# Kernel optimization log

Hardware: AMD Instinct MI355X
Metric: run time of the kernel (lower is better)

Reference implementation:

```python
import jax, jax.numpy as jnp
import numpy as np

NUM_TAGS = 128
VOCAB = 50257
SEQ_LEN = 8192
START_TAG = 0   # tag2id['<s>'] in the original
END_TAG = 1     # vocab['</s>'] in the original (code quirk; treated as end-tag id)
NEG_INF = -10000.0


def setup_inputs() -> dict:
    key = jax.random.key(0)
    k1, k2, k3 = jax.random.split(key, 3)
    x = jax.random.randint(k1, (SEQ_LEN,), 0, VOCAB)
    emit_score = jax.random.normal(k2, (VOCAB, NUM_TAGS), dtype=jnp.float32)
    transitions = jax.random.normal(k3, (NUM_TAGS, NUM_TAGS), dtype=jnp.float32)
    return {"x": x, "emit_score": emit_score, "transitions": transitions}


def reference(x, emit_score, transitions):
    # CRF forward algorithm (log partition function z).
    # Original: per-timestep, per-tag python loops of log_sum_exp over
    # _score = alphas[:, None] + emit[ch_id][None, :] + transitions.
    # All num_tags updates at step t read the *old* alphas (the in-place
    # writes only touch _score's source after it was built), so this is the
    # standard vectorized recurrence: a logsumexp reduction over the prev-tag axis.
    emits = emit_score[x[1:]]  # [S-1, T] gathered emission scores
    init_alphas = jnp.full((NUM_TAGS,), NEG_INF, dtype=emit_score.dtype).at[START_TAG].set(0.0)

    def step(alphas, emit_t):
        # score[prev, cur] = alphas[prev] + emit_t[cur] + transitions[prev, cur]
        score = alphas[:, None] + emit_t[None, :] + transitions  # [T, T]
        return jax.nn.logsumexp(score, axis=0), None

    alphas, _ = jax.lax.scan(step, init_alphas, emits)
    z = jax.nn.logsumexp(alphas + transitions[:, END_TAG])  # scalar
    return z
```

## Files before the change

### kernel.cpp

```cpp
#include <hip/hip_runtime.h>

#define NTG 128
#define NSTEPS 8191
#define GCH 512
#define LCH 16
#define MATF16 (NTG*NTG)

typedef _Float16 half8v  __attribute__((ext_vector_type(8)));
typedef _Float16 half4v  __attribute__((ext_vector_type(4)));
typedef float    float4v __attribute__((ext_vector_type(4)));

__device__ __forceinline__ int su(int row, int col){
  return (row*NTG + col) ^ ((row & 15) << 3);
}

__device__ __forceinline__ float wave_max(float v){
#pragma unroll
  for (int m = 32; m >= 1; m >>= 1) v = fmaxf(v, __shfl_xor(v, m));
  return v;
}
__device__ __forceinline__ float wave_sum(float v){
#pragma unroll
  for (int m = 32; m >= 1; m >>= 1) v += __shfl_xor(v, m);
  return v;
}

__device__ __forceinline__ float red8(const float* rg){
  const float4v r0 = *(const float4v*)rg;
  const float4v r1 = *(const float4v*)(rg+4);
  return fmaxf(fmaxf(fmaxf(r0[0],r0[1]),fmaxf(r0[2],r0[3])),
               fmaxf(fmaxf(r1[0],r1[1]),fmaxf(r1[2],r1[3])));
}

__global__ __launch_bounds__(512, 4)
void k_chunks(const int* __restrict__ x, const float* __restrict__ emit,
              const float* __restrict__ T, _Float16* __restrict__ Pt,
              double* __restrict__ scale)
{
  __shared__ _Float16 X[2][MATF16];
  __shared__ float ehl[2][NTG];
  __shared__ float red_g[2][8];

  const int t = threadIdx.x, lane = t & 63, wv = t >> 6;
  const int l15 = lane & 15, g4 = lane >> 4;
  const int wr = wv >> 1, wc = wv & 1;
  const int g = blockIdx.x, s0 = g*LCH;
  const int nst = min(LCH, NSTEPS - s0);

  half8v aE[2][4];
#pragma unroll
  for (int rt=0; rt<2; ++rt){
    const int j = wr*32 + rt*16 + l15;
#pragma unroll
    for (int ks=0; ks<4; ++ks){
      half8v a;
#pragma unroll
      for (int jj=0; jj<8; ++jj)
        a[jj] = (_Float16)__expf(T[(ks*32 + g4*8 + jj)*NTG + j]);
      aE[rt][ks] = a;
    }
  }

  int tokv = 0;
  if (wv==0) tokv = x[1 + s0 + min(lane, nst-1)];

  double cacc = 0.0;
  {
    const int tok0 = x[1+s0];
    const float2 e0 = *(const float2*)(emit + (size_t)tok0*NTG + lane*2);
    const float m0 = wave_max(fmaxf(e0.x, e0.y));
    const float sa = __expf(e0.x - m0)*0.0078125f;
    const float sb = __expf(e0.y - m0)*0.0078125f;
    const int j0 = lane*2;
#pragma unroll
    for (int it=0; it<16; ++it){
      const int idx = it*512 + t;
      const int i = idx >> 6;
      const float2 tv = *(const float2*)(T + (size_t)i*NTG + j0);
      union { unsigned u; _Float16 h[2]; } pk;
      pk.h[0] = (_Float16)(__expf(tv.x)*sa);
      pk.h[1] = (_Float16)(__expf(tv.y)*sb);
      *(unsigned*)&X[1][su(i, j0)] = pk.u;
    }
    if (t==0) cacc = (double)m0 + 4.852030263919617;
    if (wv==0){
      const int tok1 = __shfl(tokv, 1);
      const float2 e1 = *(const float2*)(emit + (size_t)tok1*NTG + lane*2);
      const float m1 = wave_max(fmaxf(e1.x, e1.y));
      *(float2*)&ehl[1][lane*2] = make_float2(__expf(e1.x-m1), __expf(e1.y-m1));
      if (t==0) cacc += (double)m1;
    }
    if (t<8) red_g[0][t] = 1.0f;
  }

  float4v accv[2][4];
  for (int s=1; s<nst; ++s){
    __syncthreads();
    const float gmax = red8(&red_g[(s-1)&1][0]);
    const float pscale = 1.0f/gmax;
    if (t==0) cacc += (double)__logf(gmax);

#pragma unroll
    for (int rt=0;rt<2;++rt)
#pragma unroll
      for (int ct=0;ct<4;++ct) accv[rt][ct] = (float4v){0.f,0.f,0.f,0.f};

    const _Float16* __restrict__ Xs = X[s&1];
#pragma unroll
    for (int ct=0; ct<4; ++ct){
      const int c = wc*64 + ct*16 + l15;
      half8v bf[4];
#pragma unroll
      for (int ks=0;ks<4;++ks)
        bf[ks] = *(const half8v*)&Xs[su(c, ks*32 + g4*8)];
#pragma unroll
      for (int rt=0;rt<2;++rt)
#pragma unroll
        for (int ks=0;ks<4;++ks)
          accv[rt][ct] = __builtin_amdgcn_mfma_f32_16x16x32_f16(aE[rt][ks], bf[ks], accv[rt][ct], 0,0,0);
    }

    if (wv==0 && s+1<nst){
      const int tokn = __shfl(tokv, s+1);
      const float2 en = *(const float2*)(emit + (size_t)tokn*NTG + lane*2);
      const float mn = wave_max(fmaxf(en.x,en.y));
      *(float2*)&ehl[(s+1)&1][lane*2] = make_float2(__expf(en.x-mn), __expf(en.y-mn));
      if (t==0) cacc += (double)mn;
    }

    float gm = 0.f;
    _Float16* __restrict__ Xd = X[(s+1)&1];
#pragma unroll
    for (int rt=0;rt<2;++rt){
      const float4v eh4 = *(const float4v*)&ehl[s&1][wr*32 + rt*16 + g4*4];
#pragma unroll
      for (int ct=0;ct<4;++ct){
        half4v h;
#pragma unroll
        for (int r=0;r<4;r++){
          const float v = accv[rt][ct][r]*eh4[r]*pscale;
          gm = fmaxf(gm, v);
          h[r] = (_Float16)v;
        }
        *(half4v*)&Xd[su(wc*64 + ct*16 + l15, wr*32 + rt*16 + g4*4)] = h;
      }
    }
    gm = wave_max(gm);
    if (lane==0) red_g[s&1][wv] = gm;
  }

  __syncthreads();
  {
    const float gmaxF = red8(&red_g[(nst-1)&1][0]);
    const float inv = 1.0f/gmaxF;
    const _Float16* __restrict__ Xf = X[nst&1];
    unsigned* pt = (unsigned*)(Pt + (size_t)g*MATF16);
#pragma unroll
    for (int it=0; it<16; ++it){
      const int uidx = it*512 + t;
      const int jj = uidx >> 6, ii = (uidx & 63)*2;
      union { unsigned u; _Float16 h[2]; } pk;
      pk.h[0] = (_Float16)((float)Xf[su(ii,   jj)]*inv);
      pk.h[1] = (_Float16)((float)Xf[su(ii+1, jj)]*inv);
      pt[uidx] = pk.u;
    }
    if (t==0) scale[g] = cacc + (double)__logf(gmaxF);
  }
}

__global__ __launch_bounds__(512, 2)
void k_comb8(const _Float16* __restrict__ Pt_in, const double* __restrict__ Sin,
             _Float16* __restrict__ Pt_out, double* __restrict__ Sout)
{
  __shared__ _Float16 X[2][MATF16];
  __shared__ float red_g[2][8];
  const int t = threadIdx.x, lane = t & 63, wv = t >> 6;
  const int l15 = lane & 15, g4 = lane >> 4;
  const int wr = wv >> 1, wc = wv & 1;
  const int p = blockIdx.x;
  const _Float16* __restrict__ base = Pt_in + (size_t)p*8*MATF16;

  {
    const unsigned* src = (const unsigned*)base;
#pragma unroll
    for (int it=0; it<16; ++it){
      const int pos = it*512 + t;
      union { unsigned u; _Float16 h[2]; } pk;
      pk.u = src[pos];
      const int jj = pos >> 6, ii = (pos & 63)*2;
      X[1][su(ii,   jj)] = pk.h[0];
      X[1][su(ii+1, jj)] = pk.h[1];
    }
    if (t<8) red_g[0][t] = 1.0f;
  }

  half8v aB[2][4];
#pragma unroll
  for (int rt=0;rt<2;++rt)
#pragma unroll
    for (int ks=0;ks<4;++ks)
      aB[rt][ks] = *(const half8v*)(base + MATF16 + (size_t)(wr*32+rt*16+l15)*NTG + ks*32 + g4*8);

  double slog = 0.0;
  float4v accv[2][4];
#pragma unroll
  for (int mi=1; mi<8; ++mi){
    __syncthreads();
    const float gmax = red8(&red_g[(mi-1)&1][0]);
    const float pscale = 1.0f/gmax;
    if (t==0) slog += (double)__logf(gmax);

#pragma unroll
    for (int rt=0;rt<2;++rt)
#pragma unroll
      for (int ct=0;ct<4;++ct) accv[rt][ct] = (float4v){0.f,0.f,0.f,0.f};

    const _Float16* __restrict__ Xs = X[mi&1];
#pragma unroll
    for (int ct=0; ct<4; ++ct){
      const int c = wc*64 + ct*16 + l15;
      half8v bf[4];
#pragma unroll
      for (int ks=0;ks<4;++ks)
        bf[ks] = *(const half8v*)&Xs[su(c, ks*32 + g4*8)];
#pragma unroll
      for (int rt=0;rt<2;++rt)
#pragma unroll
        for (int ks=0;ks<4;++ks)
          accv[rt][ct] = __builtin_amdgcn_mfma_f32_16x16x32_f16(aB[rt][ks], bf[ks], accv[rt][ct], 0,0,0);
    }

    half8v aBn[2][4];
    if (mi<7){
#pragma unroll
      for (int rt=0;rt<2;++rt)
#pragma unroll
        for (int ks=0;ks<4;++ks)
          aBn[rt][ks] = *(const half8v*)(base + (size_t)(mi+1)*MATF16 + (size_t)(wr*32+rt*16+l15)*NTG + ks*32 + g4*8);
    }

    float gm = 0.f;
    _Float16* __restrict__ Xd = X[(mi+1)&1];
#pragma unroll
    for (int rt=0;rt<2;++rt)
#pragma unroll
      for (int ct=0;ct<4;++ct){
        half4v h;
#pragma unroll
        for (int r=0;r<4;r++){
          const float v = accv[rt][ct][r]*pscale;
          gm = fmaxf(gm, v);
          h[r] = (_Float16)v;
        }
        *(half4v*)&Xd[su(wc*64 + ct*16 + l15, wr*32 + rt*16 + g4*4)] = h;
      }
    gm = wave_max(gm);
    if (lane==0) red_g[mi&1][wv] = gm;

    if (mi<7){
#pragma unroll
      for (int rt=0;rt<2;++rt)
#pragma unroll
        for (int ks=0;ks<4;++ks) aB[rt][ks] = aBn[rt][ks];
    }
  }

  __syncthreads();
  {
    const float gmaxF = red8(&red_g[1][0]);
    const float inv = 1.0f/gmaxF;
    const _Float16* __restrict__ Xf = X[0];
    unsigned* pt = (unsigned*)(Pt_out + (size_t)p*MATF16);
#pragma unroll
    for (int it=0; it<16; ++it){
      const int uidx = it*512 + t;
      const int jj = uidx >> 6, ii = (uidx & 63)*2;
      union { unsigned u; _Float16 h[2]; } pk;
      pk.h[0] = (_Float16)((float)Xf[su(ii,   jj)]*inv);
      pk.h[1] = (_Float16)((float)Xf[su(ii+1, jj)]*inv);
      pt[uidx] = pk.u;
    }
    if (t==0){
      double ssum = slog + (double)__logf(gmaxF);
#pragma unroll
      for (int q=0;q<8;q++) ssum += Sin[p*8+q];
      Sout[p] = ssum;
    }
  }
}

__global__ void k_final(const _Float16* __restrict__ PtC, const double* __restrict__ scC,
                        const float* __restrict__ T, float* __restrict__ out)
{
  __shared__ float u[2][NTG];
  __shared__ float red[4], red2[4];
  const int t = threadIdx.x;
  const int lane = t & 63, wv = t >> 6;

  double acc = 0.0;
#pragma unroll
  for (int q=0;q<8;q++) acc += scC[q];

  if (t < NTG) u[0][t] = (t==0) ? 1.f : 0.f;
  __syncthreads();

  int cur = 0;
  const int r = t >> 1, off = (t&1)*64;
  for (int k=0;k<8;k++){
    const _Float16* Y = PtC + (size_t)k*MATF16 + (size_t)r*NTG + off;
    float dot = 0.f;
#pragma unroll
    for (int q=0;q<8;q++){
      const half8v h = *(const half8v*)(Y + q*8);
#pragma unroll
      for (int e=0;e<8;e++) dot += (float)h[e]*u[cur][off + q*8 + e];
    }
    dot += __shfl_xor(dot, 1);
    if ((t&1)==0) u[cur^1][r] = dot;
    __syncthreads();
    cur ^= 1;
  }

  const float val = (t < NTG) ? (__logf(u[cur][t]) + T[t*NTG + 1]) : -3.0e38f;
  float mx = wave_max(val);
  if (lane==0) red[wv] = mx;
  __syncthreads();
  mx = fmaxf(red[0], red[1]);
  const float e = (t < NTG) ? __expf(val - mx) : 0.f;
  const float s = wave_sum(e);
  if (lane==0) red2[wv] = s;
  __syncthreads();
  if (t==0){
    const double z = (double)mx + log((double)(red2[0]+red2[1])) + acc;
    out[0] = (float)z;
  }
}

extern "C" void kernel_launch(void* const* d_in, const int* in_sizes, int n_in,
                              void* d_out, int out_size, void* d_ws, size_t ws_size,
                              hipStream_t stream)
{
  const int*   x    = (const int*)d_in[0];
  const float* emit = (const float*)d_in[1];
  const float* T    = (const float*)d_in[2];
  float* out = (float*)d_out;

  _Float16* PtA = (_Float16*)d_ws;
  _Float16* PtB = PtA + (size_t)512*MATF16;
  _Float16* PtC = PtB + (size_t)64*MATF16;
  double* scA = (double*)(PtC + (size_t)8*MATF16);
  double* scB = scA + 512;
  double* scC = scB + 64;

  k_chunks<<<GCH, 512, 0, stream>>>(x, emit, T, PtA, scA);
  k_comb8<<<64, 512, 0, stream>>>(PtA, scA, PtB, scB);
  k_comb8<<< 8, 512, 0, stream>>>(PtB, scB, PtC, scC);
  k_final<<<1, 256, 0, stream>>>(PtC, scC, T, out);
}
```

Measured before the change: 171.9 us.

## Restructure CRF scan: more shorter chunks, precomputed exp(T), single-buffer LDS, deeper final chain

Doubles the number of chunk blocks and halves steps per chunk. exp(transitions) is now computed once in a prep kernel, in normal and transposed fp16 form, instead of per block. LDS drops to a single buffer with an extra barrier, and the warp tiling changes to 2x4 so each wave holds 4 A-row tiles. Launch bounds target 8 blocks per CU. One comb8 level is removed, and the final kernel now runs a 128-step matrix-vector chain with per-step max normalization and prefetching. The aim is more parallelism and less redundant exp work, at the cost of a longer serial final reduction and an extra synchronization per step.

Measured after the change: 555.0 us. 223% more time.

```diff
diff --git a/kernel.cpp b/kernel.cpp
--- a/kernel.cpp
+++ b/kernel.cpp
@@ -2,9 +2,10 @@
 
 #define NTG 128
 #define NSTEPS 8191
-#define GCH 512
-#define LCH 16
+#define GCH 1024
+#define LCH 8
 #define MATF16 (NTG*NTG)
+#define NB1 (GCH/8)
 
 typedef _Float16 half8v  __attribute__((ext_vector_type(8)));
 typedef _Float16 half4v  __attribute__((ext_vector_type(4)));
@@ -24,7 +25,6 @@
   for (int m = 32; m >= 1; m >>= 1) v += __shfl_xor(v, m);
   return v;
 }
-
 __device__ __forceinline__ float red8(const float* rg){
   const float4v r0 = *(const float4v*)rg;
   const float4v r1 = *(const float4v*)(rg+4);
@@ -32,292 +32,302 @@
                fmaxf(fmaxf(r1[0],r1[1]),fmaxf(r1[2],r1[3])));
 }
 
-__global__ __launch_bounds__(512, 4)
+__global__ void k_prep(const float* __restrict__ T, _Float16* __restrict__ En,
+                       _Float16* __restrict__ Et){
+  const int idx = blockIdx.x*256 + threadIdx.x;
+  const int i = idx >> 7, j = idx & 127;
+  const float v = __expf(T[idx]);
+  En[idx] = (_Float16)v;
+  Et[j*NTG + i] = (_Float16)v;
+}
+
+__global__ __launch_bounds__(512, 8)
 void k_chunks(const int* __restrict__ x, const float* __restrict__ emit,
-              const float* __restrict__ T, _Float16* __restrict__ Pt,
-              double* __restrict__ scale)
+              const _Float16* __restrict__ En, const _Float16* __restrict__ Et,
+              _Float16* __restrict__ Pt, double* __restrict__ scale)
 {
-  __shared__ _Float16 X[2][MATF16];
-  __shared__ float ehl[2][NTG];
+  __shared__ _Float16 X[MATF16];
   __shared__ float red_g[2][8];
 
   const int t = threadIdx.x, lane = t & 63, wv = t >> 6;
   const int l15 = lane & 15, g4 = lane >> 4;
-  const int wr = wv >> 1, wc = wv & 1;
+  const int wr = wv >> 2, wc = wv & 3;
   const int g = blockIdx.x, s0 = g*LCH;
   const int nst = min(LCH, NSTEPS - s0);
 
-  half8v aE[2][4];
-#pragma unroll
-  for (int rt=0; rt<2; ++rt){
-    const int j = wr*32 + rt*16 + l15;
-#pragma unroll
-    for (int ks=0; ks<4; ++ks){
-      half8v a;
-#pragma unroll
-      for (int jj=0; jj<8; ++jj)
-        a[jj] = (_Float16)__expf(T[(ks*32 + g4*8 + jj)*NTG + j]);
-      aE[rt][ks] = a;
-    }
-  }
-
-  int tokv = 0;
-  if (wv==0) tokv = x[1 + s0 + min(lane, nst-1)];
+  half8v aE[4][4];
+#pragma unroll
+  for (int rt=0; rt<4; ++rt){
+    const int j = wr*64 + rt*16 + l15;
+#pragma unroll
+    for (int ks=0; ks<4; ++ks)
+      aE[rt][ks] = *(const half8v*)(Et + j*NTG + ks*32 + g4*8);
+  }
+
+  const int tokv = x[1 + s0 + min(lane & 7, nst-1)];
 
   double cacc = 0.0;
   {
-    const int tok0 = x[1+s0];
+    const int tok0 = __shfl(tokv, 0);
     const float2 e0 = *(const float2*)(emit + (size_t)tok0*NTG + lane*2);
     const float m0 = wave_max(fmaxf(e0.x, e0.y));
     const float sa = __expf(e0.x - m0)*0.0078125f;
     const float sb = __expf(e0.y - m0)*0.0078125f;
     const int j0 = lane*2;
+    const unsigned* ens = (const unsigned*)En;
 #pragma unroll
     for (int it=0; it<16; ++it){
       const int idx = it*512 + t;
       const int i = idx >> 6;
-      const float2 tv = *(const float2*)(T + (size_t)i*NTG + j0);
       union { unsigned u; _Float16 h[2]; } pk;
-      pk.h[0] = (_Float16)(__expf(tv.x)*sa);
-      pk.h[1] = (_Float16)(__expf(tv.y)*sb);
-      *(unsigned*)&X[1][su(i, j0)] = pk.u;
+      pk.u = ens[idx];
+      pk.h[0] = (_Float16)((float)pk.h[0]*sa);
+      pk.h[1] = (_Float16)((float)pk.h[1]*sb);
+      *(unsigned*)&X[su(i, j0)] = pk.u;
     }
     if (t==0) cacc = (double)m0 + 4.852030263919617;
-    if (wv==0){
-      const int tok1 = __shfl(tokv, 1);
-      const float2 e1 = *(const float2*)(emit + (size_t)tok1*NTG + lane*2);
-      const float m1 = wave_max(fmaxf(e1.x, e1.y));
-      *(float2*)&ehl[1][lane*2] = make_float2(__expf(e1.x-m1), __expf(e1.y-m1));
-      if (t==0) cacc += (double)m1;
-    }
     if (t<8) red_g[0][t] = 1.0f;
   }
-
-  float4v accv[2][4];
+  __syncthreads();
+
+  float4v accv[4][2];
   for (int s=1; s<nst; ++s){
-    __syncthreads();
-    const float gmax = red8(&red_g[(s-1)&1][0]);
-    const float pscale = 1.0f/gmax;
-    if (t==0) cacc += (double)__logf(gmax);
-
-#pragma unroll
-    for (int rt=0;rt<2;++rt)
-#pragma unroll
-      for (int ct=0;ct<4;++ct) accv[rt][ct] = (float4v){0.f,0.f,0.f,0.f};
-
-    const _Float16* __restrict__ Xs = X[s&1];
-#pragma unroll
-    for (int ct=0; ct<4; ++ct){
-      const int c = wc*64 + ct*16 + l15;
+    const int tok = __shfl(tokv, s);
+    const float* er = emit + (size_t)tok*NTG;
+    const float2 e2 = *(const float2*)(er + lane*2);
+    const float m = wave_max(fmaxf(e2.x, e2.y));
+    const float gprev = red8(&red_g[(s-1)&1][0]);
+    const float ps = 1.0f/gprev;
+    if (t==0) cacc += (double)m + (double)__logf(gprev);
+
+    float ehp[4][4];
+#pragma unroll
+    for (int rt=0; rt<4; ++rt)
+#pragma unroll
+      for (int r=0; r<4; ++r)
+        ehp[rt][r] = __expf(er[wr*64 + rt*16 + g4*4 + r] - m) * ps;
+
+#pragma unroll
+    for (int rt=0;rt<4;++rt)
+#pragma unroll
+      for (int ct=0;ct<2;++ct) accv[rt][ct] = (float4v){0.f,0.f,0.f,0.f};
+
+#pragma unroll
+    for (int ct=0; ct<2; ++ct){
+      const int c = wc*32 + ct*16 + l15;
       half8v bf[4];
 #pragma unroll
       for (int ks=0;ks<4;++ks)
-        bf[ks] = *(const half8v*)&Xs[su(c, ks*32 + g4*8)];
-#pragma unroll
-      for (int rt=0;rt<2;++rt)
+        bf[ks] = *(const half8v*)&X[su(c, ks*32 + g4*8)];
+#pragma unroll
+      for (int rt=0;rt<4;++rt)
 #pragma unroll
         for (int ks=0;ks<4;++ks)
           accv[rt][ct] = __builtin_amdgcn_mfma_f32_16x16x32_f16(aE[rt][ks], bf[ks], accv[rt][ct], 0,0,0);
     }
-
-    if (wv==0 && s+1<nst){
-      const int tokn = __shfl(tokv, s+1);
-      const float2 en = *(const float2*)(emit + (size_t)tokn*NTG + lane*2);
-      const float mn = wave_max(fmaxf(en.x,en.y));
-      *(float2*)&ehl[(s+1)&1][lane*2] = make_float2(__expf(en.x-mn), __expf(en.y-mn));
-      if (t==0) cacc += (double)mn;
-    }
+    __syncthreads();
 
     float gm = 0.f;
-    _Float16* __restrict__ Xd = X[(s+1)&1];
-#pragma unroll
-    for (int rt=0;rt<2;++rt){
-      const float4v eh4 = *(const float4v*)&ehl[s&1][wr*32 + rt*16 + g4*4];
-#pragma unroll
-      for (int ct=0;ct<4;++ct){
+#pragma unroll
+    for (int rt=0;rt<4;++rt)
+#pragma unroll
+      for (int ct=0;ct<2;++ct){
         half4v h;
 #pragma unroll
         for (int r=0;r<4;r++){
-          const float v = accv[rt][ct][r]*eh4[r]*pscale;
+          const float v = accv[rt][ct][r]*ehp[rt][r];
           gm = fmaxf(gm, v);
           h[r] = (_Float16)v;
         }
-        *(half4v*)&Xd[su(wc*64 + ct*16 + l15, wr*32 + rt*16 + g4*4)] = h;
+        *(half4v*)&X[su(wc*32 + ct*16 + l15, wr*64 + rt*16 + g4*4)] = h;
       }
-    }
     gm = wave_max(gm);
     if (lane==0) red_g[s&1][wv] = gm;
-  }
-
-  __syncthreads();
-  {
-    const float gmaxF = red8(&red_g[(nst-1)&1][0]);
-    const float inv = 1.0f/gmaxF;
-    const _Float16* __restrict__ Xf = X[nst&1];
-    unsigned* pt = (unsigned*)(Pt + (size_t)g*MATF16);
-#pragma unroll
-    for (int it=0; it<16; ++it){
-      const int uidx = it*512 + t;
-      const int jj = uidx >> 6, ii = (uidx & 63)*2;
-      union { unsigned u; _Float16 h[2]; } pk;
-      pk.h[0] = (_Float16)((float)Xf[su(ii,   jj)]*inv);
-      pk.h[1] = (_Float16)((float)Xf[su(ii+1, jj)]*inv);
-      pt[uidx] = pk.u;
-    }
-    if (t==0) scale[g] = cacc + (double)__logf(gmaxF);
-  }
+    __syncthreads();
+  }
+
+  const float gF = red8(&red_g[(nst-1)&1][0]);
+  const float inv = 1.0f/gF;
+  unsigned* pt = (unsigned*)(Pt + (size_t)g*MATF16);
+  const int ii = lane*2;
+#pragma unroll
+  for (int it=0; it<16; ++it){
+    const int uidx = it*512 + t;
+    const int jj = uidx >> 6;
+    union { unsigned u; _Float16 h[2]; } pk;
+    pk.h[0] = (_Float16)((float)X[su(ii,   jj)]*inv);
+    pk.h[1] = (_Float16)((float)X[su(ii+1, jj)]*inv);
+    pt[uidx] = pk.u;
+  }
+  if (t==0) scale[g] = cacc + (double)__logf(gF);
 }
 
 __global__ __launch_bounds__(512, 2)
 void k_comb8(const _Float16* __restrict__ Pt_in, const double* __restrict__ Sin,
              _Float16* __restrict__ Pt_out, double* __restrict__ Sout)
 {
-  __shared__ _Float16 X[2][MATF16];
+  __shared__ _Float16 X[MATF16];
   __shared__ float red_g[2][8];
   const int t = threadIdx.x, lane = t & 63, wv = t >> 6;
   const int l15 = lane & 15, g4 = lane >> 4;
-  const int wr = wv >> 1, wc = wv & 1;
+  const int wr = wv >> 2, wc = wv & 3;
   const int p = blockIdx.x;
   const _Float16* __restrict__ base = Pt_in + (size_t)p*8*MATF16;
 
   {
     const unsigned* src = (const unsigned*)base;
+    const int i0 = lane*2;
 #pragma unroll
     for (int it=0; it<16; ++it){
       const int pos = it*512 + t;
       union { unsigned u; _Float16 h[2]; } pk;
       pk.u = src[pos];
-      const int jj = pos >> 6, ii = (pos & 63)*2;
-      X[1][su(ii,   jj)] = pk.h[0];
-      X[1][su(ii+1, jj)] = pk.h[1];
+      const int jj = pos >> 6;
+      X[su(i0,   jj)] = pk.h[0];
+      X[su(i0+1, jj)] = pk.h[1];
     }
     if (t<8) red_g[0][t] = 1.0f;
   }
-
-  half8v aB[2][4];
-#pragma unroll
-  for (int rt=0;rt<2;++rt)
+  __syncthreads();
+
+  half8v aB[4][4];
+#pragma unroll
+  for (int rt=0;rt<4;++rt)
 #pragma unroll
     for (int ks=0;ks<4;++ks)
-      aB[rt][ks] = *(const half8v*)(base + MATF16 + (size_t)(wr*32+rt*16+l15)*NTG + ks*32 + g4*8);
+      aB[rt][ks] = *(const half8v*)(base + MATF16 + (size_t)(wr*64+rt*16+l15)*NTG + ks*32 + g4*8);
 
   double slog = 0.0;
-  float4v accv[2][4];
-#pragma unroll
+  float4v accv[4][2];
+#pragma unroll 1
   for (int mi=1; mi<8; ++mi){
-    __syncthreads();
-    const float gmax = red8(&red_g[(mi-1)&1][0]);
-    const float pscale = 1.0f/gmax;
-    if (t==0) slog += (double)__logf(gmax);
-
-#pragma unroll
-    for (int rt=0;rt<2;++rt)
-#pragma unroll
-      for (int ct=0;ct<4;++ct) accv[rt][ct] = (float4v){0.f,0.f,0.f,0.f};
-
-    const _Float16* __restrict__ Xs = X[mi&1];
-#pragma unroll
-    for (int ct=0; ct<4; ++ct){
-      const int c = wc*64 + ct*16 + l15;
+#pragma unroll
+    for (int rt=0;rt<4;++rt)
+#pragma unroll
+      for (int ct=0;ct<2;++ct) accv[rt][ct] = (float4v){0.f,0.f,0.f,0.f};
+
+    const _Float16* __restrict__ Xs = X;
+#pragma unroll
+    for (int ct=0; ct<2; ++ct){
+      const int c = wc*32 + ct*16 + l15;
       half8v bf[4];
 #pragma unroll
       for (int ks=0;ks<4;++ks)
         bf[ks] = *(const half8v*)&Xs[su(c, ks*32 + g4*8)];
 #pragma unroll
-      for (int rt=0;rt<2;++rt)
+      for (int rt=0;rt<4;++rt)
 #pragma unroll
         for (int ks=0;ks<4;++ks)
           accv[rt][ct] = __builtin_amdgcn_mfma_f32_16x16x32_f16(aB[rt][ks], bf[ks], accv[rt][ct], 0,0,0);
     }
 
-    half8v aBn[2][4];
+    half8v aBn[4][4];
     if (mi<7){
 #pragma unroll
-      for (int rt=0;rt<2;++rt)
+      for (int rt=0;rt<4;++rt)
 #pragma unroll
         for (int ks=0;ks<4;++ks)
-          aBn[rt][ks] = *(const half8v*)(base + (size_t)(mi+1)*MATF16 + (size_t)(wr*32+rt*16+l15)*NTG + ks*32 + g4*8);
-    }
-
+          aBn[rt][ks] = *(const half8v*)(base + (size_t)(mi+1)*MATF16 + (size_t)(wr*64+rt*16+l15)*NTG + ks*32 + g4*8);
+    }
+    __syncthreads();
+
+    const float gprev = red8(&red_g[(mi-1)&1][0]);
+    const float ps = 1.0f/gprev;
+    if (t==0) slog += (double)__logf(gprev);
     float gm = 0.f;
-    _Float16* __restrict__ Xd = X[(mi+1)&1];
-#pragma unroll
-    for (int rt=0;rt<2;++rt)
-#pragma unroll
-      for (int ct=0;ct<4;++ct){
+#pragma unroll
+    for (int rt=0;rt<4;++rt)
+#pragma unroll
+      for (int ct=0;ct<2;++ct){
         half4v h;
 #pragma unroll
         for (int r=0;r<4;r++){
-          const float v = accv[rt][ct][r]*pscale;
+          const float v = accv[rt][ct][r]*ps;
           gm = fmaxf(gm, v);
           h[r] = (_Float16)v;
         }
-        *(half4v*)&Xd[su(wc*64 + ct*16 + l15, wr*32 + rt*16 + g4*4)] = h;
+        *(half4v*)&X[su(wc*32 + ct*16 + l15, wr*64 + rt*16 + g4*4)] = h;
       }
     gm = wave_max(gm);
     if (lane==0) red_g[mi&1][wv] = gm;
+    __syncthreads();
 
     if (mi<7){
 #pragma unroll
-      for (int rt=0;rt<2;++rt)
+      for (int rt=0;rt<4;++rt)
 #pragma unroll
         for (int ks=0;ks<4;++ks) aB[rt][ks] = aBn[rt][ks];
     }
   }
 
-  __syncthreads();
-  {
-    const float gmaxF = red8(&red_g[1][0]);
-    const float inv = 1.0f/gmaxF;
-    const _Float16* __restrict__ Xf = X[0];
-    unsigned* pt = (unsigned*)(Pt_out + (size_t)p*MATF16);
-#pragma unroll
-    for (int it=0; it<16; ++it){
-      const int uidx = it*512 + t;
-      const int jj = uidx >> 6, ii = (uidx & 63)*2;
-      union { unsigned u; _Float16 h[2]; } pk;
-      pk.h[0] = (_Float16)((float)Xf[su(ii,   jj)]*inv);
-      pk.h[1] = (_Float16)((float)Xf[su(ii+1, jj)]*inv);
-      pt[uidx] = pk.u;
-    }
-    if (t==0){
-      double ssum = slog + (double)__logf(gmaxF);
-#pragma unroll
-      for (int q=0;q<8;q++) ssum += Sin[p*8+q];
-      Sout[p] = ssum;
-    }
-  }
-}
-
-__global__ void k_final(const _Float16* __restrict__ PtC, const double* __restrict__ scC,
+  const float gF = red8(&red_g[1][0]);
+  const float inv = 1.0f/gF;
+  unsigned* pt = (unsigned*)(Pt_out + (size_t)p*MATF16);
+  const int ii = lane*2;
+#pragma unroll
+  for (int it=0; it<16; ++it){
+    const int uidx = it*512 + t;
+    const int jj = uidx >> 6;
+    union { unsigned u; _Float16 h[2]; } pk;
+    pk.h[0] = (_Float16)((float)X[su(ii,   jj)]*inv);
+    pk.h[1] = (_Float16)((float)X[su(ii+1, jj)]*inv);
+    pt[uidx] = pk.u;
+  }
+  if (t==0){
+    double ssum = slog + (double)__logf(gF);
+#pragma unroll
+    for (int q=0;q<8;q++) ssum += Sin[p*8+q];
+    Sout[p] = ssum;
+  }
+}
+
+__global__ void k_final(const _Float16* __restrict__ PtB, const double* __restrict__ scB,
                         const float* __restrict__ T, float* __restrict__ out)
 {
   __shared__ float u[2][NTG];
-  __shared__ float red[4], red2[4];
-  const int t = threadIdx.x;
-  const int lane = t & 63, wv = t >> 6;
-
-  double acc = 0.0;
-#pragma unroll
-  for (int q=0;q<8;q++) acc += scC[q];
-
-  if (t < NTG) u[0][t] = (t==0) ? 1.f : 0.f;
-  __syncthreads();
-
+  __shared__ double sredd[8];
+  __shared__ float red[8], red2[8];
+  const int t = threadIdx.x, lane = t & 63, wv = t >> 6;
+
+  double ss = (t < NB1) ? scB[t] : 0.0;
+#pragma unroll
+  for (int m=32; m>=1; m>>=1) ss += __shfl_xor(ss, m);
+  if (lane==0) sredd[wv] = ss;
+
+  if (t < NTG) u[0][t] = (t==0) ? 1.0f : 0.0f;
+
+  const int row = t >> 2, q = t & 3;
+  const _Float16* base = PtB + (size_t)row*NTG + q*32;
+  half8v cb[4], nb[4];
+#pragma unroll
+  for (int v=0; v<4; ++v) cb[v] = *(const half8v*)(base + v*8);
+  __syncthreads();
+
+  double lacc = 0.0;
   int cur = 0;
-  const int r = t >> 1, off = (t&1)*64;
-  for (int k=0;k<8;k++){
-    const _Float16* Y = PtC + (size_t)k*MATF16 + (size_t)r*NTG + off;
-    float dot = 0.f;
-#pragma unroll
-    for (int q=0;q<8;q++){
-      const half8v h = *(const half8v*)(Y + q*8);
-#pragma unroll
-      for (int e=0;e<8;e++) dot += (float)h[e]*u[cur][off + q*8 + e];
-    }
-    dot += __shfl_xor(dot, 1);
-    if ((t&1)==0) u[cur^1][r] = dot;
-    __syncthreads();
+  for (int k=0; k<NB1; ++k){
+    if (k+1 < NB1){
+      const _Float16* nx = base + (size_t)(k+1)*MATF16;
+#pragma unroll
+      for (int v=0; v<4; ++v) nb[v] = *(const half8v*)(nx + v*8);
+    }
+    float dot = 0.f, mloc = 0.f;
+#pragma unroll
+    for (int v=0; v<4; ++v)
+#pragma unroll
+      for (int e=0; e<8; ++e){
+        const float uv = u[cur][q*32 + v*8 + e];
+        dot  = fmaf((float)cb[v][e], uv, dot);
+        mloc = fmaxf(mloc, uv);
+      }
+    dot += __shfl_xor(dot, 1);  dot += __shfl_xor(dot, 2);
+    mloc = fmaxf(mloc, __shfl_xor(mloc, 1));
+    mloc = fmaxf(mloc, __shfl_xor(mloc, 2));
+    if (q==0) u[cur^1][row] = dot / mloc;
+    if (t==0) lacc += (double)__logf(mloc);
+    __syncthreads();
+#pragma unroll
+    for (int v=0; v<4; ++v) cb[v] = nb[v];
     cur ^= 1;
   }
 
@@ -325,14 +335,20 @@
   float mx = wave_max(val);
   if (lane==0) red[wv] = mx;
   __syncthreads();
-  mx = fmaxf(red[0], red[1]);
+  mx = fmaxf(fmaxf(fmaxf(red[0],red[1]),fmaxf(red[2],red[3])),
+             fmaxf(fmaxf(red[4],red[5]),fmaxf(red[6],red[7])));
   const float e = (t < NTG) ? __expf(val - mx) : 0.f;
-  const float s = wave_sum(e);
-  if (lane==0) red2[wv] = s;
+  const float sE = wave_sum(e);
+  if (lane==0) red2[wv] = sE;
   __syncthreads();
   if (t==0){
-    const double z = (double)mx + log((double)(red2[0]+red2[1])) + acc;
-    out[0] = (float)z;
+    float sumE = 0.f;
+#pragma unroll
+    for (int q2=0;q2<8;q2++) sumE += red2[q2];
+    double ssum = 0.0;
+#pragma unroll
+    for (int q2=0;q2<8;q2++) ssum += sredd[q2];
+    out[0] = (float)((double)mx + log((double)sumE) + lacc + ssum);
   }
 }
 
@@ -345,15 +361,15 @@
   const float* T    = (const float*)d_in[2];
   float* out = (float*)d_out;
 
-  _Float16* PtA = (_Float16*)d_ws;
-  _Float16* PtB = PtA + (size_t)512*MATF16;
-  _Float16* PtC = PtB + (size_t)64*MATF16;
-  double* scA = (double*)(PtC + (size_t)8*MATF16);
-  double* scB = scA + 512;
-  double* scC = scB + 64;
-
-  k_chunks<<<GCH, 512, 0, stream>>>(x, emit, T, PtA, scA);
-  k_comb8<<<64, 512, 0, stream>>>(PtA, scA, PtB, scB);
-  k_comb8<<< 8, 512, 0, stream>>>(PtB, scB, PtC, scC);
-  k_final<<<1, 256, 0, stream>>>(PtC, scC, T, out);
-}
+  _Float16* En  = (_Float16*)d_ws;
+  _Float16* Et  = En  + MATF16;
+  _Float16* PtA = Et  + MATF16;
+  _Float16* PtB = PtA + (size_t)GCH*MATF16;
+  double* scA = (double*)(PtB + (size_t)NB1*MATF16);
+  double* scB = scA + GCH;
+
+  k_prep<<<64, 256, 0, stream>>>(T, En, Et);
+  k_chunks<<<GCH, 512, 0, stream>>>(x, emit, En, Et, PtA, scA);
+  k_comb8<<<NB1, 512, 0, stream>>>(PtA, scA, PtB, scB);
+  k_final<<<1, 512, 0, stream>>>(PtB, scB, T, out);
+}
```
